# Kernel optimization log

Hardware: AMD Instinct MI355X
Metric: run time of the kernel (lower is better)

## Reference

```python
import jax, jax.numpy as jnp
from jax import lax
import numpy as np

B, T, NCLS, D = 64, 2048, 20, 2048
LCS_LEN, FSD_LEN = 64, 32
LAMB1, LAMB2, LAMB3 = 1.0, 5e-5, 8e-5
LAMB_LCS, LAMB_FSD = 0.01, 0.01
FEAT_MARGIN = 50.0
THRES = 0.5
GAMMA = 0.1


def cos_sim(a, b):
    a = a / jnp.linalg.norm(a, axis=1, keepdims=True)
    b = b / jnp.linalg.norm(b, axis=1, keepdims=True)
    return a @ b.T


def dp_fsd(c0, c1):
    # soft-LCS/DTW-style recurrence with maxGamma (soft max) over 3 neighbors
    h = c0.shape[-1] // 2
    m = cos_sim(c0[:, :h], c1[:, :h])  # [L, L]
    g = cos_sim(c0[:, h:], c1[:, h:])  # [L, L]
    L = m.shape[0]

    def row_step(prev_row, mg):
        m_row, g_row = mg
        diag = prev_row[:-1]  # C[i-1, j-1]
        up = prev_row[1:]     # C[i-1, j]

        def col_step(left, xs):  # left = C[i, j-1]
            d, u, mij, gij = xs
            neigh = jnp.stack([d, gij + u, gij + left])
            val = mij + GAMMA * jax.nn.logsumexp(neigh / GAMMA)
            return val, val

        _, row_vals = lax.scan(col_step, jnp.zeros((), m.dtype), (diag, up, m_row, g_row))
        new_row = jnp.concatenate([jnp.zeros((1,), m.dtype), row_vals])
        return new_row, None

    final_row, _ = lax.scan(row_step, jnp.zeros(L + 1, m.dtype), (m, g))
    return final_row[-1]


def dp_lcs(c0, c1):
    s = cos_sim(c0, c1)  # [L, L]
    L = s.shape[0]

    def row_step(prev_row, s_row):
        diag = prev_row[:-1]
        up = prev_row[1:]

        def col_step(left, xs):
            d, u, sij = xs
            val = jnp.where(sij > THRES, d + sij, jnp.maximum(u, left))
            return val, val

        _, row_vals = lax.scan(col_step, jnp.zeros((), s.dtype), (diag, up, s_row))
        return jnp.concatenate([jnp.zeros((1,), s.dtype), row_vals]), None

    final_row, _ = lax.scan(row_step, jnp.zeros(L + 1, s.dtype), s)
    return final_row[-1]


def cls_criterion(p, lab):
    return -jnp.mean(jnp.sum(jnp.log(p + 1e-10) * lab, axis=1))


def forward_once(ai_cls, ac_cls, ab_cls, vlab, att, ai_feat, ac_feat, ab_feat, ai_cas):
    bs = ai_cls.shape[0]
    ones = jnp.ones((bs, 1), ai_cls.dtype)
    zeros = jnp.zeros((bs, 1), ai_cls.dtype)
    inst_lab = jnp.concatenate([vlab, zeros], axis=1)
    cont_lab = jnp.concatenate([vlab, ones], axis=1)
    back_lab = jnp.concatenate([jnp.zeros_like(vlab), ones], axis=1)
    inst_lab = inst_lab / jnp.sum(inst_lab, axis=1, keepdims=True)
    cont_lab = cont_lab / jnp.sum(cont_lab, axis=1, keepdims=True)
    back_lab = back_lab / jnp.sum(back_lab, axis=1, keepdims=True)

    inst_loss = cls_criterion(ai_cls, inst_lab)
    cont_loss = cls_criterion(ac_cls, cont_lab)
    back_loss = cls_criterion(ab_cls, back_lab)

    guide_loss = jnp.mean(jnp.sum(jnp.abs(1.0 - ai_cas[:, :, -1] - lax.stop_gradient(att[:, :, 0])), axis=1))

    n_inst = jnp.linalg.norm(ai_feat, axis=1)
    n_cont = jnp.linalg.norm(ac_feat, axis=1)
    n_back = jnp.linalg.norm(ab_feat, axis=1)
    f1 = jnp.maximum(FEAT_MARGIN - n_inst + n_cont, 0.0)
    f2 = jnp.maximum(FEAT_MARGIN - n_cont + n_back, 0.0)
    f3 = n_back
    feat_loss = jnp.mean((f1 + f2 + f3) ** 2)

    sparse_loss = jnp.mean(jnp.sum(att[:, :, :2], axis=1))

    cls_loss = inst_loss + cont_loss + back_loss  # THUMOS14 weights 1/1/1
    return cls_loss + LAMB1 * guide_loss + LAMB2 * feat_loss + LAMB3 * sparse_loss


def _pair_loss(vals, pair_label):
    bs = vals.shape[0]
    pos = jnp.sum(vals * pair_label)
    neg = jnp.sum(vals * (1.0 - pair_label))
    pos_num = jnp.sum(pair_label)
    neg_num = bs - pos_num
    return neg / (neg_num + 1e-10) - pos / (pos_num + 1e-10)


def ftcl_forward(act_inst_cls_0, act_cont_cls_0, act_back_cls_0, vid_label_0, temp_att_0,
                 act_inst_feat_0, act_cont_feat_0, act_back_feat_0, act_inst_cas_0,
                 lcs_candi_0, fsd_act_candi_0, fsd_bak_candi_0,
                 act_inst_cls_1, act_cont_cls_1, act_back_cls_1, vid_label_1, temp_att_1,
                 act_inst_feat_1, act_cont_feat_1, act_back_feat_1, act_inst_cas_1,
                 lcs_candi_1, fsd_act_candi_1, fsd_bak_candi_1):
    loss_0 = forward_once(act_inst_cls_0, act_cont_cls_0, act_back_cls_0, vid_label_0, temp_att_0,
                          act_inst_feat_0, act_cont_feat_0, act_back_feat_0, act_inst_cas_0)
    loss_1 = forward_once(act_inst_cls_1, act_cont_cls_1, act_back_cls_1, vid_label_1, temp_att_1,
                          act_inst_feat_1, act_cont_feat_1, act_back_feat_1, act_inst_cas_1)
    acm_loss = (loss_0 + loss_1) / 2.0

    pair_label = (jnp.sum(vid_label_0 * vid_label_1, axis=1) > 0).astype(jnp.float32)  # [B]

    lcs = jax.vmap(dp_lcs)(lcs_candi_0, lcs_candi_1)  # [B]
    lcs_loss = _pair_loss(lcs, pair_label)

    # pair==1 -> act_1, pair==0 -> bak_1 (matches the per-sample branch in torch)
    fsd_c1 = jnp.where(pair_label[:, None, None] > 0, fsd_act_candi_1, fsd_bak_candi_1)
    fsd = jax.vmap(dp_fsd)(fsd_act_candi_0, fsd_c1)  # [B]
    fsd_loss = _pair_loss(fsd, pair_label)

    return acm_loss + LAMB_LCS * lcs_loss + LAMB_FSD * fsd_loss


def setup_inputs() -> dict:
    key = jax.random.key(0)
    ks = iter(jax.random.split(key, 32))
    rand = lambda s: jax.random.uniform(next(ks), s, jnp.float32)
    randn = lambda s: jax.random.normal(next(ks), s, jnp.float32)
    inp = {}
    for sfx in ('0', '1'):
        inp[f'act_inst_cls_{sfx}'] = rand((B, NCLS + 1))
        inp[f'act_cont_cls_{sfx}'] = rand((B, NCLS + 1))
        inp[f'act_back_cls_{sfx}'] = rand((B, NCLS + 1))
        inp[f'vid_label_{sfx}'] = jnp.ones((B, NCLS), jnp.float32)
        inp[f'temp_att_{sfx}'] = rand((B, T, 3))
        inp[f'act_inst_feat_{sfx}'] = randn((B, D))
        inp[f'act_cont_feat_{sfx}'] = randn((B, D))
        inp[f'act_back_feat_{sfx}'] = randn((B, D))
        inp[f'act_inst_cas_{sfx}'] = rand((B, T, NCLS + 1))
        inp[f'lcs_candi_{sfx}'] = randn((B, LCS_LEN, D))
        inp[f'fsd_act_candi_{sfx}'] = randn((B, FSD_LEN, D))
        inp[f'fsd_bak_candi_{sfx}'] = randn((B, FSD_LEN, D))
    return inp


def reference(act_inst_cls_0, act_cont_cls_0, act_back_cls_0, vid_label_0, temp_att_0,
              act_inst_feat_0, act_cont_feat_0, act_back_feat_0, act_inst_cas_0,
              lcs_candi_0, fsd_act_candi_0, fsd_bak_candi_0,
              act_inst_cls_1, act_cont_cls_1, act_back_cls_1, vid_label_1, temp_att_1,
              act_inst_feat_1, act_cont_feat_1, act_back_feat_1, act_inst_cas_1,
              lcs_candi_1, fsd_act_candi_1, fsd_bak_candi_1):
    return ftcl_forward(act_inst_cls_0, act_cont_cls_0, act_back_cls_0, vid_label_0, temp_att_0,
                        act_inst_feat_0, act_cont_feat_0, act_back_feat_0, act_inst_cas_0,
                        lcs_candi_0, fsd_act_candi_0, fsd_bak_candi_0,
                        act_inst_cls_1, act_cont_cls_1, act_back_cls_1, vid_label_1, temp_att_1,
                        act_inst_feat_1, act_cont_feat_1, act_back_feat_1, act_inst_cas_1,
                        lcs_candi_1, fsd_act_candi_1, fsd_bak_candi_1)
```

## Files before the change

kernel.cpp:

```cpp
#include <hip/hip_runtime.h>
#include <math.h>

#define Bn 64
#define Tn 2048
#define NCLS 20
#define Dn 2048
#define LCSL 64
#define FSDL 32

typedef __bf16 bf16x4 __attribute__((ext_vector_type(4)));
typedef __bf16 bf16x8 __attribute__((ext_vector_type(8)));
typedef float f32x4 __attribute__((ext_vector_type(4)));

#define WS_LCS 0
#define WS_FSD 64
#define WS_NORM 128
#define WS_GS 512
template <int NS>
struct WsOff {
    static constexpr size_t LSQ = 1024;
    static constexpr size_t FSQ = LSQ + (size_t)64 * NS * 128;
    static constexpr size_t SPART = FSQ + (size_t)64 * NS * 64;
    static constexpr size_t MG = SPART + (size_t)64 * NS * 4096;
    static constexpr size_t END = MG + (size_t)64 * NS * 1024;
};

template <int NS>
__global__ __launch_bounds__(256) void mega_kernel(
    const float* __restrict__ lcs0, const float* __restrict__ lcs1,
    const float* __restrict__ fA0, const float* __restrict__ fA1,
    const float* __restrict__ fB1,
    const float* __restrict__ vid0, const float* __restrict__ vid1,
    const float* __restrict__ cas0, const float* __restrict__ att0,
    const float* __restrict__ cas1, const float* __restrict__ att1,
    const float* __restrict__ f0, const float* __restrict__ f1,
    const float* __restrict__ f2, const float* __restrict__ f3,
    const float* __restrict__ f4, const float* __restrict__ f5,
    float* __restrict__ ws) {
    constexpr int L = (NS == 16) ? 4 : 3;
    constexpr int KC = 2048 / NS / 64;
    using O = WsOff<NS>;
    __shared__ __align__(16) __bf16 tA[2][4096];
    __shared__ __align__(16) __bf16 tB[2][4096];
    const int t = threadIdx.x;
    const int bid = blockIdx.x;
    const int w = t >> 6, lane = t & 63;
    const int quad = lane >> 4, l16 = lane & 15;

    if (bid < 64 * NS) {
        const int b = bid >> L, ks = bid & (NS - 1);
        const float* c0 = lcs0 + (size_t)b * LCSL * Dn + ks * (2048 / NS);
        const float* c1 = lcs1 + (size_t)b * LCSL * Dn + ks * (2048 / NS);

        f32x4 acc[4] = {};
        float sqa[4] = {0.f, 0.f, 0.f, 0.f}, sqb[4] = {0.f, 0.f, 0.f, 0.f};
        float4 pA[4], pB[4];

        auto LOADL = [&](int st) {
            #pragma unroll
            for (int l = 0; l < 4; ++l) {
                int idx4 = l * 256 + t;
                int row = idx4 >> 4, kq4 = idx4 & 15;
                pA[l] = *(const float4*)(c0 + (size_t)row * Dn + st * 64 + kq4 * 4);
                pB[l] = *(const float4*)(c1 + (size_t)row * Dn + st * 64 + kq4 * 4);
            }
        };
        auto WRITEL = [&](int buf) {
            #pragma unroll
            for (int l = 0; l < 4; ++l) {
                int idx4 = l * 256 + t;
                int row = idx4 >> 4, kq4 = idx4 & 15;
                int c = kq4 >> 1, h = kq4 & 1;
                int pos = row * 64 + ((c ^ (row & 7)) << 3) + h * 4;
                float4 av = pA[l], bv = pB[l];
                bf16x4 a4 = {(__bf16)av.x, (__bf16)av.y, (__bf16)av.z, (__bf16)av.w};
                bf16x4 b4 = {(__bf16)bv.x, (__bf16)bv.y, (__bf16)bv.z, (__bf16)bv.w};
                *(bf16x4*)&tA[buf][pos] = a4;
                *(bf16x4*)&tB[buf][pos] = b4;
                sqa[l] += av.x * av.x + av.y * av.y + av.z * av.z + av.w * av.w;
                sqb[l] += bv.x * bv.x + bv.y * bv.y + bv.z * bv.z + bv.w * bv.w;
            }
        };

        LOADL(0);
        WRITEL(0);
        if (KC > 1) LOADL(1);
        __syncthreads();
        for (int kc = 0; kc < KC; ++kc) {
            const int cur = kc & 1;
            #pragma unroll
            for (int s = 0; s < 2; ++s) {
                int ar = w * 16 + l16;
                int ac_ = (s * 4 + quad) ^ (ar & 7);
                bf16x8 af = *(const bf16x8*)&tA[cur][ar * 64 + (ac_ << 3)];
                #pragma unroll
                for (int tj = 0; tj < 4; ++tj) {
                    int br = tj * 16 + l16;
                    int bc = (s * 4 + quad) ^ (br & 7);
                    bf16x8 bf = *(const bf16x8*)&tB[cur][br * 64 + (bc << 3)];
                    acc[tj] = __builtin_amdgcn_mfma_f32_16x16x32_bf16(af, bf, acc[tj], 0, 0, 0);
                }
            }
            if (kc + 1 < KC) {
                WRITEL(cur ^ 1);
                if (kc + 2 < KC) LOADL(kc + 2);
                __syncthreads();
            }
        }
        float* dst = ws + O::SPART + (size_t)(b * NS + ks) * 4096;
        #pragma unroll
        for (int tj = 0; tj < 4; ++tj)
            #pragma unroll
            for (int rg = 0; rg < 4; ++rg)
                dst[(w * 16 + quad * 4 + rg) * 64 + tj * 16 + l16] = acc[tj][rg];
        #pragma unroll
        for (int l = 0; l < 4; ++l) {
            float sa = sqa[l], sb = sqb[l];
            #pragma unroll
            for (int m = 1; m < 16; m <<= 1) {
                sa += __shfl_xor(sa, m);
                sb += __shfl_xor(sb, m);
            }
            if ((t & 15) == 0) {
                int r = l * 16 + (t >> 4);
                float* q = ws + O::LSQ + (size_t)(b * NS + ks) * 128;
                q[r] = sa;
                q[64 + r] = sb;
            }
        }
    } else if (bid < 128 * NS) {
        const int qb = bid - 64 * NS;
        const int b = qb >> L;
        const int idx = qb & (NS - 1);
        const int half = idx >> (L - 1);
        const int ks = idx & (NS / 2 - 1);
        float ps = 0.f;
        for (int c = 0; c < NCLS; ++c) ps += vid0[b * NCLS + c] * vid1[b * NCLS + c];
        const float* base1 = (ps > 0.f) ? fA1 : fB1;
        const float* c0 = fA0 + (size_t)b * FSDL * Dn + half * 1024 + ks * (2048 / NS);
        const float* c1 = base1 + (size_t)b * FSDL * Dn + half * 1024 + ks * (2048 / NS);
        const int wi = w >> 1, wj = w & 1;

        f32x4 acc = {};
        float sqa[2] = {0.f, 0.f}, sqb[2] = {0.f, 0.f};
        float4 pA[2], pB[2];

        auto LOADF = [&](int st) {
            #pragma unroll
            for (int l = 0; l < 2; ++l) {
                int idx4 = l * 256 + t;
                int row = idx4 >> 4, kq4 = idx4 & 15;
                pA[l] = *(const float4*)(c0 + (size_t)row * Dn + st * 64 + kq4 * 4);
                pB[l] = *(const float4*)(c1 + (size_t)row * Dn + st * 64 + kq4 * 4);
            }
        };
        auto WRITEF = [&](int buf) {
            #pragma unroll
            for (int l = 0; l < 2; ++l) {
                int idx4 = l * 256 + t;
                int row = idx4 >> 4, kq4 = idx4 & 15;
                int c = kq4 >> 1, h = kq4 & 1;
                int pos = row * 64 + ((c ^ (row & 7)) << 3) + h * 4;
                float4 av = pA[l], bv = pB[l];
                bf16x4 a4 = {(__bf16)av.x, (__bf16)av.y, (__bf16)av.z, (__bf16)av.w};
                bf16x4 b4 = {(__bf16)bv.x, (__bf16)bv.y, (__bf16)bv.z, (__bf16)bv.w};
                *(bf16x4*)&tA[buf][pos] = a4;
                *(bf16x4*)&tB[buf][pos] = b4;
                sqa[l] += av.x * av.x + av.y * av.y + av.z * av.z + av.w * av.w;
                sqb[l] += bv.x * bv.x + bv.y * bv.y + bv.z * bv.z + bv.w * bv.w;
            }
        };

        LOADF(0);
        WRITEF(0);
        if (KC > 1) LOADF(1);
        __syncthreads();
        for (int kc = 0; kc < KC; ++kc) {
            const int cur = kc & 1;
            #pragma unroll
            for (int s = 0; s < 2; ++s) {
                int ar = wi * 16 + l16;
                int ac_ = (s * 4 + quad) ^ (ar & 7);
                bf16x8 af = *(const bf16x8*)&tA[cur][ar * 64 + (ac_ << 3)];
                int br = wj * 16 + l16;
                int bc = (s * 4 + quad) ^ (br & 7);
                bf16x8 bf = *(const bf16x8*)&tB[cur][br * 64 + (bc << 3)];
                acc = __builtin_amdgcn_mfma_f32_16x16x32_bf16(af, bf, acc, 0, 0, 0);
            }
            if (kc + 1 < KC) {
                WRITEF(cur ^ 1);
                if (kc + 2 < KC) LOADF(kc + 2);
                __syncthreads();
            }
        }
        float* dst = ws + O::MG + (size_t)((b * 2 + half) * (NS / 2) + ks) * 1024;
        #pragma unroll
        for (int rg = 0; rg < 4; ++rg)
            dst[(wi * 16 + quad * 4 + rg) * 32 + wj * 16 + l16] = acc[rg];
        #pragma unroll
        for (int l = 0; l < 2; ++l) {
            float sa = sqa[l], sb = sqb[l];
            #pragma unroll
            for (int m = 1; m < 16; m <<= 1) {
                sa += __shfl_xor(sa, m);
                sb += __shfl_xor(sb, m);
            }
            if ((t & 15) == 0) {
                int r = l * 16 + (t >> 4);
                float* qq = ws + O::FSQ + (size_t)((b * 2 + half) * (NS / 2) + ks) * 64;
                qq[r] = sa;
                qq[32 + r] = sb;
            }
        }
    } else if (bid < 128 * NS + 128) {
        const int gb = bid - 128 * NS;
        const int N = Bn * Tn;
        float g0 = 0.f, s0 = 0.f, g1 = 0.f, s1 = 0.f;
        for (int n = gb * 256 + t; n < 2 * N; n += 128 * 256) {
            int sfx = (n >= N);
            int m = sfx ? (n - N) : n;
            const float* cas = sfx ? cas1 : cas0;
            const float* att = sfx ? att1 : att0;
            float a0 = att[m * 3 + 0];
            float a1 = att[m * 3 + 1];
            float g = fabsf(1.0f - cas[m * (NCLS + 1) + NCLS] - a0);
            float s = a0 + a1;
            if (sfx) { g1 += g; s1 += s; } else { g0 += g; s0 += s; }
        }
        float* red = (float*)tA;
        float vals[4] = {g0, s0, g1, s1};
        #pragma unroll
        for (int v = 0; v < 4; ++v) red[v * 256 + t] = vals[v];
        __syncthreads();
        for (int o = 128; o; o >>= 1) {
            if (t < o) {
                #pragma unroll
                for (int v = 0; v < 4; ++v) red[v * 256 + t] += red[v * 256 + t + o];
            }
            __syncthreads();
        }
        if (t < 4) ws[WS_GS + gb * 4 + t] = red[t * 256];
    } else {
        int R = (bid - (128 * NS + 128)) * 4 + w;
        const float* arr[6] = {f0, f1, f2, f3, f4, f5};
        const float* p = arr[R >> 6] + (size_t)(R & 63) * Dn;
        float s = 0.f;
        #pragma unroll
        for (int qd = 0; qd < 8; ++qd) {
            float4 v = *(const float4*)(p + qd * 256 + lane * 4);
            s += v.x * v.x + v.y * v.y + v.z * v.z + v.w * v.w;
        }
        for (int off = 32; off; off >>= 1) s += __shfl_down(s, off);
        if (lane == 0) ws[WS_NORM + R] = sqrtf(s);
    }
}

template <int NS>
__global__ __launch_bounds__(256) void dp_kernel(float* __restrict__ ws) {
    using O = WsOff<NS>;
    const int t = threadIdx.x;
    if (blockIdx.x < 64) {
        const int b = blockIdx.x;
        __shared__ float S[64 * 68];
        __shared__ float inv[128];
        if (t < 128) {
            float s = 0.f;
            #pragma unroll
            for (int ks = 0; ks < NS; ++ks)
                s += ws[O::LSQ + (size_t)(b * NS + ks) * 128 + t];
            inv[t] = 1.0f / sqrtf(s);
        }
        __syncthreads();
        const float* sp = ws + O::SPART + (size_t)b * NS * 4096;
        #pragma unroll
        for (int qd = 0; qd < 4; ++qd) {
            int idx4 = qd * 256 + t;
            int i = idx4 >> 4, j = (idx4 & 15) * 4;
            float4 v = {0.f, 0.f, 0.f, 0.f};
            #pragma unroll
            for (int ks = 0; ks < NS; ++ks) {
                float4 p = *(const float4*)(sp + (size_t)ks * 4096 + idx4 * 4);
                v.x += p.x; v.y += p.y; v.z += p.z; v.w += p.w;
            }
            float ri = inv[i];
            S[i * 68 + j + 0] = v.x * ri * inv[64 + j + 0];
            S[i * 68 + j + 1] = v.y * ri * inv[64 + j + 1];
            S[i * 68 + j + 2] = v.z * ri * inv[64 + j + 2];
            S[i * 68 + j + 3] = v.w * ri * inv[64 + j + 3];
        }
        __syncthreads();
        if (t < 64) {
            float prev = 0.f, prevprev = 0.f;
            float sval_next = S[t * 68 + 0];
            for (int d = 2; d <= 128; ++d) {
                float s = sval_next;
                int jn = d - t - 1;
                if (jn >= 0 && jn < 64) sval_next = S[t * 68 + jn];
                float up = __shfl_up(prev, 1);
                float dg = __shfl_up(prevprev, 1);
                if (t == 0) { up = 0.f; dg = 0.f; }
                int j = d - t - 1;
                float left = prev;
                float val = (s > 0.5f) ? (dg + s) : fmaxf(up, left);
                float cur = (j >= 1 && j <= 64) ? val : 0.f;
                prevprev = prev;
                prev = cur;
            }
            if (t == 63) ws[WS_LCS + b] = prev;
        }
    } else {
        const int b = blockIdx.x - 64;
        __shared__ float M[32 * 36], G[32 * 36];
        __shared__ float inv[128];
        if (t < 128) {
            int half = t >> 6, sub = t & 63;
            float s = 0.f;
            #pragma unroll
            for (int ks = 0; ks < NS / 2; ++ks)
                s += ws[O::FSQ + (size_t)((b * 2 + half) * (NS / 2) + ks) * 64 + sub];
            inv[t] = 1.0f / sqrtf(s);
        }
        __syncthreads();
        {
            int idx4 = t;
            int i = idx4 >> 3, j = (idx4 & 7) * 4;
            float4 vM = {0.f, 0.f, 0.f, 0.f}, vG = {0.f, 0.f, 0.f, 0.f};
            #pragma unroll
            for (int ks = 0; ks < NS / 2; ++ks) {
                float4 pM = *(const float4*)(ws + O::MG + (size_t)((b * 2 + 0) * (NS / 2) + ks) * 1024 + idx4 * 4);
                float4 pG = *(const float4*)(ws + O::MG + (size_t)((b * 2 + 1) * (NS / 2) + ks) * 1024 + idx4 * 4);
                vM.x += pM.x; vM.y += pM.y; vM.z += pM.z; vM.w += pM.w;
                vG.x += pG.x; vG.y += pG.y; vG.z += pG.z; vG.w += pG.w;
            }
            float riM = inv[i], riG = inv[64 + i];
            M[i * 36 + j + 0] = vM.x * riM * inv[32 + j + 0];
            M[i * 36 + j + 1] = vM.y * riM * inv[32 + j + 1];
            M[i * 36 + j + 2] = vM.z * riM * inv[32 + j + 2];
            M[i * 36 + j + 3] = vM.w * riM * inv[32 + j + 3];
            G[i * 36 + j + 0] = vG.x * riG * inv[96 + j + 0];
            G[i * 36 + j + 1] = vG.y * riG * inv[96 + j + 1];
            G[i * 36 + j + 2] = vG.z * riG * inv[96 + j + 2];
            G[i * 36 + j + 3] = vG.w * riG * inv[96 + j + 3];
        }
        __syncthreads();
        if (t < 32) {
            float prev = 0.f, prevprev = 0.f;
            float m_next = M[t * 36 + 0], g_next = G[t * 36 + 0];
            for (int d = 2; d <= 64; ++d) {
                float m = m_next, g = g_next;
                int jn = d - t - 1;
                if (jn >= 0 && jn < 32) { m_next = M[t * 36 + jn]; g_next = G[t * 36 + jn]; }
                float up = __shfl_up(prev, 1);
                float dg = __shfl_up(prevprev, 1);
                if (t == 0) { up = 0.f; dg = 0.f; }
                int j = d - t - 1;
                float left = prev;
                float x0 = dg * 10.0f;
                float x1 = (g + up) * 10.0f;
                float x2 = (g + left) * 10.0f;
                float mx = fmaxf(x0, fmaxf(x1, x2));
                float lse = mx + __logf(__expf(x0 - mx) + __expf(x1 - mx) + __expf(x2 - mx));
                float val = m + 0.1f * lse;
                float cur = (j >= 1 && j <= 32) ? val : 0.f;
                prevprev = prev;
                prev = cur;
            }
            if (t == 31) ws[WS_FSD + b] = prev;
        }
    }
}

__device__ __forceinline__ float4 block_reduce4(float4 v, float4* red, int t) {
    red[t] = v;
    __syncthreads();
    for (int o = 128; o; o >>= 1) {
        if (t < o) {
            red[t].x += red[t + o].x;
            red[t].y += red[t + o].y;
            red[t].z += red[t + o].z;
            red[t].w += red[t + o].w;
        }
        __syncthreads();
    }
    float4 r = red[0];
    __syncthreads();
    return r;
}

__global__ __launch_bounds__(256) void final_kernel(
    const float* __restrict__ ai0, const float* __restrict__ ac0,
    const float* __restrict__ ab0, const float* __restrict__ vid0,
    const float* __restrict__ ai1, const float* __restrict__ ac1,
    const float* __restrict__ ab1, const float* __restrict__ vid1,
    const float* __restrict__ ws, float* __restrict__ out) {
    __shared__ float rs0[Bn], rs1[Bn], plsh[Bn];
    __shared__ __align__(16) float4 red[256];
    int t = threadIdx.x;
    if (t < Bn) {
        float s0 = 0.f, s1 = 0.f, pp = 0.f;
        for (int c = 0; c < NCLS; ++c) {
            float a = vid0[t * NCLS + c], bl = vid1[t * NCLS + c];
            s0 += a; s1 += bl; pp += a * bl;
        }
        rs0[t] = s0;
        rs1[t] = s1;
        plsh[t] = (pp > 0.f) ? 1.f : 0.f;
    }
    __syncthreads();

    float inst0 = 0.f, cont0 = 0.f, back0 = 0.f;
    float inst1 = 0.f, cont1 = 0.f, back1 = 0.f;
    for (int idx = t; idx < Bn * (NCLS + 1); idx += 256) {
        int b = idx / (NCLS + 1), c = idx % (NCLS + 1);
        float v0 = (c < NCLS) ? vid0[b * NCLS + c] : 0.f;
        float v1 = (c < NCLS) ? vid1[b * NCLS + c] : 0.f;
        float wI0 = (c < NCLS) ? (v0 / rs0[b]) : 0.f;
        float wC0 = ((c < NCLS) ? v0 : 1.f) / (rs0[b] + 1.f);
        float wI1 = (c < NCLS) ? (v1 / rs1[b]) : 0.f;
        float wC1 = ((c < NCLS) ? v1 : 1.f) / (rs1[b] + 1.f);
        inst0 += logf(ai0[idx] + 1e-10f) * wI0;
        cont0 += logf(ac0[idx] + 1e-10f) * wC0;
        inst1 += logf(ai1[idx] + 1e-10f) * wI1;
        cont1 += logf(ac1[idx] + 1e-10f) * wC1;
        if (c == NCLS) {
            back0 += logf(ab0[idx] + 1e-10f);
            back1 += logf(ab1[idx] + 1e-10f);
        }
    }

    float g0 = 0.f, s0v = 0.f, g1 = 0.f, s1v = 0.f;
    for (int i = t; i < 128; i += 256) {
        g0  += ws[WS_GS + i * 4 + 0];
        s0v += ws[WS_GS + i * 4 + 1];
        g1  += ws[WS_GS + i * 4 + 2];
        s1v += ws[WS_GS + i * 4 + 3];
    }

    float fv0 = 0.f, fv1 = 0.f;
    if (t < Bn) {
        const float* nm = ws + WS_NORM;
        {
            float ni = nm[0 * Bn + t], nc = nm[1 * Bn + t], nb = nm[2 * Bn + t];
            float f1 = fmaxf(50.0f - ni + nc, 0.f);
            float f2 = fmaxf(50.0f - nc + nb, 0.f);
            float f = f1 + f2 + nb;
            fv0 = f * f;
        }
        {
            float ni = nm[3 * Bn + t], nc = nm[4 * Bn + t], nb = nm[5 * Bn + t];
            float f1 = fmaxf(50.0f - ni + nc, 0.f);
            float f2 = fmaxf(50.0f - nc + nb, 0.f);
            float f = f1 + f2 + nb;
            fv1 = f * f;
        }
    }

    float posL = 0.f, negL = 0.f, posF = 0.f, negF = 0.f, pln = 0.f;
    if (t < Bn) {
        float pl = plsh[t];
        float lv = ws[WS_LCS + t];
        float fv = ws[WS_FSD + t];
        posL = lv * pl; negL = lv * (1.f - pl);
        posF = fv * pl; negF = fv * (1.f - pl);
        pln = pl;
    }

    float4 r1 = block_reduce4({inst0, cont0, back0, inst1}, red, t);
    float4 r2 = block_reduce4({cont1, back1, g0, s0v}, red, t);
    float4 r3 = block_reduce4({g1, s1v, fv0, fv1}, red, t);
    float4 r4 = block_reduce4({posL, negL, posF, negF}, red, t);
    float4 r5 = block_reduce4({pln, 0.f, 0.f, 0.f}, red, t);

    if (t == 0) {
        float cls0 = -(r1.x + r1.y + r1.z) / (float)Bn;
        float cls1 = -(r1.w + r2.x + r2.y) / (float)Bn;
        float guide0 = r2.z / (float)Bn;
        float sparse0 = r2.w / (float)(Bn * 2);
        float guide1 = r3.x / (float)Bn;
        float sparse1 = r3.y / (float)(Bn * 2);
        float sFeat0 = r3.z / (float)Bn;
        float sFeat1 = r3.w / (float)Bn;
        float loss0 = cls0 + 1.0f * guide0 + 5e-05f * sFeat0 + 8e-05f * sparse0;
        float loss1 = cls1 + 1.0f * guide1 + 5e-05f * sFeat1 + 8e-05f * sparse1;
        float acm = 0.5f * (loss0 + loss1);
        float posn = r5.x;
        float negn = (float)Bn - posn;
        float lcs_loss = r4.y / (negn + 1e-10f) - r4.x / (posn + 1e-10f);
        float fsd_loss = r4.w / (negn + 1e-10f) - r4.z / (posn + 1e-10f);
        out[0] = acm + 0.01f * lcs_loss + 0.01f * fsd_loss;
    }
}

extern "C" void kernel_launch(void* const* d_in, const int* in_sizes, int n_in,
                              void* d_out, int out_size, void* d_ws, size_t ws_size,
                              hipStream_t stream) {
    (void)in_sizes; (void)n_in; (void)out_size;
    const float* ai0  = (const float*)d_in[0];
    const float* ac0  = (const float*)d_in[1];
    const float* ab0  = (const float*)d_in[2];
    const float* vid0 = (const float*)d_in[3];
    const float* att0 = (const float*)d_in[4];
    const float* fi0  = (const float*)d_in[5];
    const float* fc0  = (const float*)d_in[6];
    const float* fb0  = (const float*)d_in[7];
    const float* cas0 = (const float*)d_in[8];
    const float* lcs0 = (const float*)d_in[9];
    const float* fsdA0 = (const float*)d_in[10];
    const float* ai1  = (const float*)d_in[12];
    const float* ac1  = (const float*)d_in[13];
    const float* ab1  = (const float*)d_in[14];
    const float* vid1 = (const float*)d_in[15];
    const float* att1 = (const float*)d_in[16];
    const float* fi1  = (const float*)d_in[17];
    const float* fc1  = (const float*)d_in[18];
    const float* fb1  = (const float*)d_in[19];
    const float* cas1 = (const float*)d_in[20];
    const float* lcs1 = (const float*)d_in[21];
    const float* fsdA1 = (const float*)d_in[22];
    const float* fsdB1 = (const float*)d_in[23];

    float* ws = (float*)d_ws;

    if (ws_size >= WsOff<16>::END * sizeof(float)) {
        mega_kernel<16><<<128 * 16 + 224, 256, 0, stream>>>(
            lcs0, lcs1, fsdA0, fsdA1, fsdB1, vid0, vid1, cas0, att0, cas1, att1,
            fi0, fc0, fb0, fi1, fc1, fb1, ws);
        dp_kernel<16><<<128, 256, 0, stream>>>(ws);
    } else {
        mega_kernel<8><<<128 * 8 + 224, 256, 0, stream>>>(
            lcs0, lcs1, fsdA0, fsdA1, fsdB1, vid0, vid1, cas0, att0, cas1, att1,
            fi0, fc0, fb0, fi1, fc1, fb1, ws);
        dp_kernel<8><<<128, 256, 0, stream>>>(ws);
    }
    final_kernel<<<1, 256, 0, stream>>>(ai0, ac0, ab0, vid0, ai1, ac1, ab1, vid1, ws,
                                        (float*)d_out);
}
```

Before: 236.0 us.

## Fuse DP into mega kernel with one block per batch, dropping split-K partials

Replaces the split-K scheme (many blocks writing partial similarity tiles to workspace, then a separate dp_kernel reducing them) with one 512-thread block per batch item. Each block computes the full-K similarity GEMM, normalizes it, and runs the DP recurrence in-block. This removes one kernel launch and the workspace round trip for the partial sums. The cost is far less parallelism: 304 blocks instead of over 2000, each looping over the full K dimension, and the FSD path leaves half its waves idle during the MFMA loop. The final kernel's block reductions also switch to wave shuffles.

```diff
diff --git a/kernel.cpp b/kernel.cpp
--- a/kernel.cpp
+++ b/kernel.cpp
@@ -16,17 +16,11 @@
 #define WS_FSD 64
 #define WS_NORM 128
 #define WS_GS 512
-template <int NS>
-struct WsOff {
-    static constexpr size_t LSQ = 1024;
-    static constexpr size_t FSQ = LSQ + (size_t)64 * NS * 128;
-    static constexpr size_t SPART = FSQ + (size_t)64 * NS * 64;
-    static constexpr size_t MG = SPART + (size_t)64 * NS * 4096;
-    static constexpr size_t END = MG + (size_t)64 * NS * 1024;
-};
-
-template <int NS>
-__global__ __launch_bounds__(256) void mega_kernel(
+
+#define AUXB 176
+#define NBLK 304
+
+__global__ __launch_bounds__(512) void mega_kernel(
     const float* __restrict__ lcs0, const float* __restrict__ lcs1,
     const float* __restrict__ fA0, const float* __restrict__ fA1,
     const float* __restrict__ fB1,
@@ -37,29 +31,69 @@
     const float* __restrict__ f2, const float* __restrict__ f3,
     const float* __restrict__ f4, const float* __restrict__ f5,
     float* __restrict__ ws) {
-    constexpr int L = (NS == 16) ? 4 : 3;
-    constexpr int KC = 2048 / NS / 64;
-    using O = WsOff<NS>;
     __shared__ __align__(16) __bf16 tA[2][4096];
     __shared__ __align__(16) __bf16 tB[2][4096];
+    __shared__ __align__(16) float S[64 * 68];
+    __shared__ float inv[128];
     const int t = threadIdx.x;
     const int bid = blockIdx.x;
     const int w = t >> 6, lane = t & 63;
     const int quad = lane >> 4, l16 = lane & 15;
 
-    if (bid < 64 * NS) {
-        const int b = bid >> L, ks = bid & (NS - 1);
-        const float* c0 = lcs0 + (size_t)b * LCSL * Dn + ks * (2048 / NS);
-        const float* c1 = lcs1 + (size_t)b * LCSL * Dn + ks * (2048 / NS);
-
-        f32x4 acc[4] = {};
-        float sqa[4] = {0.f, 0.f, 0.f, 0.f}, sqb[4] = {0.f, 0.f, 0.f, 0.f};
-        float4 pA[4], pB[4];
+    if (bid < 128) {
+        const int gb = bid;
+        const int N = Bn * Tn;
+        float g0 = 0.f, s0 = 0.f, g1 = 0.f, s1 = 0.f;
+        for (int n = gb * 512 + t; n < 2 * N; n += 128 * 512) {
+            int sfx = (n >= N);
+            int m = sfx ? (n - N) : n;
+            const float* cas = sfx ? cas1 : cas0;
+            const float* att = sfx ? att1 : att0;
+            float a0 = att[m * 3 + 0];
+            float a1 = att[m * 3 + 1];
+            float g = fabsf(1.0f - cas[m * (NCLS + 1) + NCLS] - a0);
+            float s = a0 + a1;
+            if (sfx) { g1 += g; s1 += s; } else { g0 += g; s0 += s; }
+        }
+        float* red = S;
+        float vals[4] = {g0, s0, g1, s1};
+        #pragma unroll
+        for (int v = 0; v < 4; ++v) red[v * 512 + t] = vals[v];
+        __syncthreads();
+        for (int o = 256; o; o >>= 1) {
+            if (t < o) {
+                #pragma unroll
+                for (int v = 0; v < 4; ++v) red[v * 512 + t] += red[v * 512 + t + o];
+            }
+            __syncthreads();
+        }
+        if (t < 4) ws[WS_GS + gb * 4 + t] = red[t * 512];
+    } else if (bid < AUXB) {
+        int R = (bid - 128) * 8 + w;
+        const float* arr[6] = {f0, f1, f2, f3, f4, f5};
+        const float* p = arr[R >> 6] + (size_t)(R & 63) * Dn;
+        float s = 0.f;
+        #pragma unroll
+        for (int qd = 0; qd < 8; ++qd) {
+            float4 v = *(const float4*)(p + qd * 256 + lane * 4);
+            s += v.x * v.x + v.y * v.y + v.z * v.z + v.w * v.w;
+        }
+        for (int off = 32; off; off >>= 1) s += __shfl_down(s, off);
+        if (lane == 0) ws[WS_NORM + R] = sqrtf(s);
+    } else if (bid < 240) {
+        const int b = bid - AUXB;
+        const float* c0 = lcs0 + (size_t)b * LCSL * Dn;
+        const float* c1 = lcs1 + (size_t)b * LCSL * Dn;
+        constexpr int KC = 32;
+
+        f32x4 acc[2] = {};
+        float sqa[2] = {0.f, 0.f}, sqb[2] = {0.f, 0.f};
+        float4 pA[2], pB[2];
 
         auto LOADL = [&](int st) {
             #pragma unroll
-            for (int l = 0; l < 4; ++l) {
-                int idx4 = l * 256 + t;
+            for (int l = 0; l < 2; ++l) {
+                int idx4 = l * 512 + t;
                 int row = idx4 >> 4, kq4 = idx4 & 15;
                 pA[l] = *(const float4*)(c0 + (size_t)row * Dn + st * 64 + kq4 * 4);
                 pB[l] = *(const float4*)(c1 + (size_t)row * Dn + st * 64 + kq4 * 4);
@@ -67,8 +101,8 @@
         };
         auto WRITEL = [&](int buf) {
             #pragma unroll
-            for (int l = 0; l < 4; ++l) {
-                int idx4 = l * 256 + t;
+            for (int l = 0; l < 2; ++l) {
+                int idx4 = l * 512 + t;
                 int row = idx4 >> 4, kq4 = idx4 & 15;
                 int c = kq4 >> 1, h = kq4 & 1;
                 int pos = row * 64 + ((c ^ (row & 7)) << 3) + h * 4;
@@ -84,18 +118,18 @@
 
         LOADL(0);
         WRITEL(0);
-        if (KC > 1) LOADL(1);
+        LOADL(1);
         __syncthreads();
         for (int kc = 0; kc < KC; ++kc) {
             const int cur = kc & 1;
             #pragma unroll
             for (int s = 0; s < 2; ++s) {
-                int ar = w * 16 + l16;
+                int ar = (w >> 1) * 16 + l16;
                 int ac_ = (s * 4 + quad) ^ (ar & 7);
                 bf16x8 af = *(const bf16x8*)&tA[cur][ar * 64 + (ac_ << 3)];
                 #pragma unroll
-                for (int tj = 0; tj < 4; ++tj) {
-                    int br = tj * 16 + l16;
+                for (int tj = 0; tj < 2; ++tj) {
+                    int br = (w & 1) * 32 + tj * 16 + l16;
                     int bc = (s * 4 + quad) ^ (br & 7);
                     bf16x8 bf = *(const bf16x8*)&tB[cur][br * 64 + (bc << 3)];
                     acc[tj] = __builtin_amdgcn_mfma_f32_16x16x32_bf16(af, bf, acc[tj], 0, 0, 0);
@@ -107,96 +141,6 @@
                 __syncthreads();
             }
         }
-        float* dst = ws + O::SPART + (size_t)(b * NS + ks) * 4096;
-        #pragma unroll
-        for (int tj = 0; tj < 4; ++tj)
-            #pragma unroll
-            for (int rg = 0; rg < 4; ++rg)
-                dst[(w * 16 + quad * 4 + rg) * 64 + tj * 16 + l16] = acc[tj][rg];
-        #pragma unroll
-        for (int l = 0; l < 4; ++l) {
-            float sa = sqa[l], sb = sqb[l];
-            #pragma unroll
-            for (int m = 1; m < 16; m <<= 1) {
-                sa += __shfl_xor(sa, m);
-                sb += __shfl_xor(sb, m);
-            }
-            if ((t & 15) == 0) {
-                int r = l * 16 + (t >> 4);
-                float* q = ws + O::LSQ + (size_t)(b * NS + ks) * 128;
-                q[r] = sa;
-                q[64 + r] = sb;
-            }
-        }
-    } else if (bid < 128 * NS) {
-        const int qb = bid - 64 * NS;
-        const int b = qb >> L;
-        const int idx = qb & (NS - 1);
-        const int half = idx >> (L - 1);
-        const int ks = idx & (NS / 2 - 1);
-        float ps = 0.f;
-        for (int c = 0; c < NCLS; ++c) ps += vid0[b * NCLS + c] * vid1[b * NCLS + c];
-        const float* base1 = (ps > 0.f) ? fA1 : fB1;
-        const float* c0 = fA0 + (size_t)b * FSDL * Dn + half * 1024 + ks * (2048 / NS);
-        const float* c1 = base1 + (size_t)b * FSDL * Dn + half * 1024 + ks * (2048 / NS);
-        const int wi = w >> 1, wj = w & 1;
-
-        f32x4 acc = {};
-        float sqa[2] = {0.f, 0.f}, sqb[2] = {0.f, 0.f};
-        float4 pA[2], pB[2];
-
-        auto LOADF = [&](int st) {
-            #pragma unroll
-            for (int l = 0; l < 2; ++l) {
-                int idx4 = l * 256 + t;
-                int row = idx4 >> 4, kq4 = idx4 & 15;
-                pA[l] = *(const float4*)(c0 + (size_t)row * Dn + st * 64 + kq4 * 4);
-                pB[l] = *(const float4*)(c1 + (size_t)row * Dn + st * 64 + kq4 * 4);
-            }
-        };
-        auto WRITEF = [&](int buf) {
-            #pragma unroll
-            for (int l = 0; l < 2; ++l) {
-                int idx4 = l * 256 + t;
-                int row = idx4 >> 4, kq4 = idx4 & 15;
-                int c = kq4 >> 1, h = kq4 & 1;
-                int pos = row * 64 + ((c ^ (row & 7)) << 3) + h * 4;
-                float4 av = pA[l], bv = pB[l];
-                bf16x4 a4 = {(__bf16)av.x, (__bf16)av.y, (__bf16)av.z, (__bf16)av.w};
-                bf16x4 b4 = {(__bf16)bv.x, (__bf16)bv.y, (__bf16)bv.z, (__bf16)bv.w};
-                *(bf16x4*)&tA[buf][pos] = a4;
-                *(bf16x4*)&tB[buf][pos] = b4;
-                sqa[l] += av.x * av.x + av.y * av.y + av.z * av.z + av.w * av.w;
-                sqb[l] += bv.x * bv.x + bv.y * bv.y + bv.z * bv.z + bv.w * bv.w;
-            }
-        };
-
-        LOADF(0);
-        WRITEF(0);
-        if (KC > 1) LOADF(1);
-        __syncthreads();
-        for (int kc = 0; kc < KC; ++kc) {
-            const int cur = kc & 1;
-            #pragma unroll
-            for (int s = 0; s < 2; ++s) {
-                int ar = wi * 16 + l16;
-                int ac_ = (s * 4 + quad) ^ (ar & 7);
-                bf16x8 af = *(const bf16x8*)&tA[cur][ar * 64 + (ac_ << 3)];
-                int br = wj * 16 + l16;
-                int bc = (s * 4 + quad) ^ (br & 7);
-                bf16x8 bf = *(const bf16x8*)&tB[cur][br * 64 + (bc << 3)];
-                acc = __builtin_amdgcn_mfma_f32_16x16x32_bf16(af, bf, acc, 0, 0, 0);
-            }
-            if (kc + 1 < KC) {
-                WRITEF(cur ^ 1);
-                if (kc + 2 < KC) LOADF(kc + 2);
-                __syncthreads();
-            }
-        }
-        float* dst = ws + O::MG + (size_t)((b * 2 + half) * (NS / 2) + ks) * 1024;
-        #pragma unroll
-        for (int rg = 0; rg < 4; ++rg)
-            dst[(wi * 16 + quad * 4 + rg) * 32 + wj * 16 + l16] = acc[rg];
         #pragma unroll
         for (int l = 0; l < 2; ++l) {
             float sa = sqa[l], sb = sqb[l];
@@ -206,88 +150,22 @@
                 sb += __shfl_xor(sb, m);
             }
             if ((t & 15) == 0) {
-                int r = l * 16 + (t >> 4);
-                float* qq = ws + O::FSQ + (size_t)((b * 2 + half) * (NS / 2) + ks) * 64;
-                qq[r] = sa;
-                qq[32 + r] = sb;
-            }
-        }
-    } else if (bid < 128 * NS + 128) {
-        const int gb = bid - 128 * NS;
-        const int N = Bn * Tn;
-        float g0 = 0.f, s0 = 0.f, g1 = 0.f, s1 = 0.f;
-        for (int n = gb * 256 + t; n < 2 * N; n += 128 * 256) {
-            int sfx = (n >= N);
-            int m = sfx ? (n - N) : n;
-            const float* cas = sfx ? cas1 : cas0;
-            const float* att = sfx ? att1 : att0;
-            float a0 = att[m * 3 + 0];
-            float a1 = att[m * 3 + 1];
-            float g = fabsf(1.0f - cas[m * (NCLS + 1) + NCLS] - a0);
-            float s = a0 + a1;
-            if (sfx) { g1 += g; s1 += s; } else { g0 += g; s0 += s; }
-        }
-        float* red = (float*)tA;
-        float vals[4] = {g0, s0, g1, s1};
+                int r = l * 32 + (t >> 4);
+                inv[r] = sa;
+                inv[64 + r] = sb;
+            }
+        }
+        __syncthreads();
+        if (t < 128) inv[t] = 1.0f / sqrtf(inv[t]);
+        __syncthreads();
         #pragma unroll
-        for (int v = 0; v < 4; ++v) red[v * 256 + t] = vals[v];
-        __syncthreads();
-        for (int o = 128; o; o >>= 1) {
-            if (t < o) {
-                #pragma unroll
-                for (int v = 0; v < 4; ++v) red[v * 256 + t] += red[v * 256 + t + o];
-            }
-            __syncthreads();
-        }
-        if (t < 4) ws[WS_GS + gb * 4 + t] = red[t * 256];
-    } else {
-        int R = (bid - (128 * NS + 128)) * 4 + w;
-        const float* arr[6] = {f0, f1, f2, f3, f4, f5};
-        const float* p = arr[R >> 6] + (size_t)(R & 63) * Dn;
-        float s = 0.f;
-        #pragma unroll
-        for (int qd = 0; qd < 8; ++qd) {
-            float4 v = *(const float4*)(p + qd * 256 + lane * 4);
-            s += v.x * v.x + v.y * v.y + v.z * v.z + v.w * v.w;
-        }
-        for (int off = 32; off; off >>= 1) s += __shfl_down(s, off);
-        if (lane == 0) ws[WS_NORM + R] = sqrtf(s);
-    }
-}
-
-template <int NS>
-__global__ __launch_bounds__(256) void dp_kernel(float* __restrict__ ws) {
-    using O = WsOff<NS>;
-    const int t = threadIdx.x;
-    if (blockIdx.x < 64) {
-        const int b = blockIdx.x;
-        __shared__ float S[64 * 68];
-        __shared__ float inv[128];
-        if (t < 128) {
-            float s = 0.f;
+        for (int tj = 0; tj < 2; ++tj)
             #pragma unroll
-            for (int ks = 0; ks < NS; ++ks)
-                s += ws[O::LSQ + (size_t)(b * NS + ks) * 128 + t];
-            inv[t] = 1.0f / sqrtf(s);
-        }
-        __syncthreads();
-        const float* sp = ws + O::SPART + (size_t)b * NS * 4096;
-        #pragma unroll
-        for (int qd = 0; qd < 4; ++qd) {
-            int idx4 = qd * 256 + t;
-            int i = idx4 >> 4, j = (idx4 & 15) * 4;
-            float4 v = {0.f, 0.f, 0.f, 0.f};
-            #pragma unroll
-            for (int ks = 0; ks < NS; ++ks) {
-                float4 p = *(const float4*)(sp + (size_t)ks * 4096 + idx4 * 4);
-                v.x += p.x; v.y += p.y; v.z += p.z; v.w += p.w;
-            }
-            float ri = inv[i];
-            S[i * 68 + j + 0] = v.x * ri * inv[64 + j + 0];
-            S[i * 68 + j + 1] = v.y * ri * inv[64 + j + 1];
-            S[i * 68 + j + 2] = v.z * ri * inv[64 + j + 2];
-            S[i * 68 + j + 3] = v.w * ri * inv[64 + j + 3];
-        }
+            for (int rg = 0; rg < 4; ++rg) {
+                int row = (w >> 1) * 16 + quad * 4 + rg;
+                int col = (w & 1) * 32 + tj * 16 + l16;
+                S[row * 68 + col] = acc[tj][rg] * inv[row] * inv[64 + col];
+            }
         __syncthreads();
         if (t < 64) {
             float prev = 0.f, prevprev = 0.f;
@@ -309,47 +187,98 @@
             if (t == 63) ws[WS_LCS + b] = prev;
         }
     } else {
-        const int b = blockIdx.x - 64;
-        __shared__ float M[32 * 36], G[32 * 36];
-        __shared__ float inv[128];
-        if (t < 128) {
-            int half = t >> 6, sub = t & 63;
-            float s = 0.f;
-            #pragma unroll
-            for (int ks = 0; ks < NS / 2; ++ks)
-                s += ws[O::FSQ + (size_t)((b * 2 + half) * (NS / 2) + ks) * 64 + sub];
-            inv[t] = 1.0f / sqrtf(s);
-        }
-        __syncthreads();
-        {
-            int idx4 = t;
-            int i = idx4 >> 3, j = (idx4 & 7) * 4;
-            float4 vM = {0.f, 0.f, 0.f, 0.f}, vG = {0.f, 0.f, 0.f, 0.f};
-            #pragma unroll
-            for (int ks = 0; ks < NS / 2; ++ks) {
-                float4 pM = *(const float4*)(ws + O::MG + (size_t)((b * 2 + 0) * (NS / 2) + ks) * 1024 + idx4 * 4);
-                float4 pG = *(const float4*)(ws + O::MG + (size_t)((b * 2 + 1) * (NS / 2) + ks) * 1024 + idx4 * 4);
-                vM.x += pM.x; vM.y += pM.y; vM.z += pM.z; vM.w += pM.w;
-                vG.x += pG.x; vG.y += pG.y; vG.z += pG.z; vG.w += pG.w;
-            }
-            float riM = inv[i], riG = inv[64 + i];
-            M[i * 36 + j + 0] = vM.x * riM * inv[32 + j + 0];
-            M[i * 36 + j + 1] = vM.y * riM * inv[32 + j + 1];
-            M[i * 36 + j + 2] = vM.z * riM * inv[32 + j + 2];
-            M[i * 36 + j + 3] = vM.w * riM * inv[32 + j + 3];
-            G[i * 36 + j + 0] = vG.x * riG * inv[96 + j + 0];
-            G[i * 36 + j + 1] = vG.y * riG * inv[96 + j + 1];
-            G[i * 36 + j + 2] = vG.z * riG * inv[96 + j + 2];
-            G[i * 36 + j + 3] = vG.w * riG * inv[96 + j + 3];
-        }
-        __syncthreads();
+        const int b = bid - 240;
+        float ps = 0.f;
+        for (int c = 0; c < NCLS; ++c) ps += vid0[b * NCLS + c] * vid1[b * NCLS + c];
+        const float* base1 = (ps > 0.f) ? fA1 : fB1;
+        const float* c0 = fA0 + (size_t)b * FSDL * Dn;
+        const float* c1 = base1 + (size_t)b * FSDL * Dn;
+        const int wi = w >> 1, wj = w & 1;
+        float* Ml = S;
+        float* Gl = S + 1152;
+        constexpr int KC = 16;
+
+        for (int ph = 0; ph < 2; ++ph) {
+            const int off = ph * 1024;
+            f32x4 acc = {};
+            float sqa = 0.f, sqb = 0.f;
+            float4 pA, pB;
+            auto LOADF = [&](int st) {
+                int row = t >> 4, kq4 = t & 15;
+                pA = *(const float4*)(c0 + (size_t)row * Dn + off + st * 64 + kq4 * 4);
+                pB = *(const float4*)(c1 + (size_t)row * Dn + off + st * 64 + kq4 * 4);
+            };
+            auto WRITEF = [&](int buf) {
+                int row = t >> 4, kq4 = t & 15;
+                int c = kq4 >> 1, h = kq4 & 1;
+                int pos = row * 64 + ((c ^ (row & 7)) << 3) + h * 4;
+                float4 av = pA, bv = pB;
+                bf16x4 a4 = {(__bf16)av.x, (__bf16)av.y, (__bf16)av.z, (__bf16)av.w};
+                bf16x4 b4 = {(__bf16)bv.x, (__bf16)bv.y, (__bf16)bv.z, (__bf16)bv.w};
+                *(bf16x4*)&tA[buf][pos] = a4;
+                *(bf16x4*)&tB[buf][pos] = b4;
+                sqa += av.x * av.x + av.y * av.y + av.z * av.z + av.w * av.w;
+                sqb += bv.x * bv.x + bv.y * bv.y + bv.z * bv.z + bv.w * bv.w;
+            };
+
+            LOADF(0);
+            WRITEF(0);
+            LOADF(1);
+            __syncthreads();
+            for (int kc = 0; kc < KC; ++kc) {
+                const int cur = kc & 1;
+                if (w < 4) {
+                    #pragma unroll
+                    for (int s = 0; s < 2; ++s) {
+                        int ar = wi * 16 + l16;
+                        int ac_ = (s * 4 + quad) ^ (ar & 7);
+                        bf16x8 af = *(const bf16x8*)&tA[cur][ar * 64 + (ac_ << 3)];
+                        int br = wj * 16 + l16;
+                        int bc = (s * 4 + quad) ^ (br & 7);
+                        bf16x8 bf = *(const bf16x8*)&tB[cur][br * 64 + (bc << 3)];
+                        acc = __builtin_amdgcn_mfma_f32_16x16x32_bf16(af, bf, acc, 0, 0, 0);
+                    }
+                }
+                if (kc + 1 < KC) {
+                    WRITEF(cur ^ 1);
+                    if (kc + 2 < KC) LOADF(kc + 2);
+                    __syncthreads();
+                }
+            }
+            {
+                float sa = sqa, sb = sqb;
+                #pragma unroll
+                for (int m = 1; m < 16; m <<= 1) {
+                    sa += __shfl_xor(sa, m);
+                    sb += __shfl_xor(sb, m);
+                }
+                if ((t & 15) == 0) {
+                    int r = t >> 4;
+                    inv[r] = sa;
+                    inv[32 + r] = sb;
+                }
+            }
+            __syncthreads();
+            if (t < 64) inv[t] = 1.0f / sqrtf(inv[t]);
+            __syncthreads();
+            if (w < 4) {
+                float* T = (ph == 0) ? Ml : Gl;
+                #pragma unroll
+                for (int rg = 0; rg < 4; ++rg) {
+                    int row = wi * 16 + quad * 4 + rg;
+                    int col = wj * 16 + l16;
+                    T[row * 36 + col] = acc[rg] * inv[row] * inv[32 + col];
+                }
+            }
+            __syncthreads();
+        }
         if (t < 32) {
             float prev = 0.f, prevprev = 0.f;
-            float m_next = M[t * 36 + 0], g_next = G[t * 36 + 0];
+            float m_next = Ml[t * 36 + 0], g_next = Gl[t * 36 + 0];
             for (int d = 2; d <= 64; ++d) {
                 float m = m_next, g = g_next;
                 int jn = d - t - 1;
-                if (jn >= 0 && jn < 32) { m_next = M[t * 36 + jn]; g_next = G[t * 36 + jn]; }
+                if (jn >= 0 && jn < 32) { m_next = Ml[t * 36 + jn]; g_next = Gl[t * 36 + jn]; }
                 float up = __shfl_up(prev, 1);
                 float dg = __shfl_up(prevprev, 1);
                 if (t == 0) { up = 0.f; dg = 0.f; }
@@ -370,19 +299,21 @@
     }
 }
 
-__device__ __forceinline__ float4 block_reduce4(float4 v, float4* red, int t) {
-    red[t] = v;
+__device__ __forceinline__ float4 wbr4(float4 v, float4* redw, int t) {
+    #pragma unroll
+    for (int m = 1; m < 64; m <<= 1) {
+        v.x += __shfl_xor(v.x, m);
+        v.y += __shfl_xor(v.y, m);
+        v.z += __shfl_xor(v.z, m);
+        v.w += __shfl_xor(v.w, m);
+    }
+    if ((t & 63) == 0) redw[t >> 6] = v;
     __syncthreads();
-    for (int o = 128; o; o >>= 1) {
-        if (t < o) {
-            red[t].x += red[t + o].x;
-            red[t].y += red[t + o].y;
-            red[t].z += red[t + o].z;
-            red[t].w += red[t + o].w;
-        }
-        __syncthreads();
-    }
-    float4 r = red[0];
+    float4 r;
+    r.x = redw[0].x + redw[1].x + redw[2].x + redw[3].x;
+    r.y = redw[0].y + redw[1].y + redw[2].y + redw[3].y;
+    r.z = redw[0].z + redw[1].z + redw[2].z + redw[3].z;
+    r.w = redw[0].w + redw[1].w + redw[2].w + redw[3].w;
     __syncthreads();
     return r;
 }
@@ -394,7 +325,7 @@
     const float* __restrict__ ab1, const float* __restrict__ vid1,
     const float* __restrict__ ws, float* __restrict__ out) {
     __shared__ float rs0[Bn], rs1[Bn], plsh[Bn];
-    __shared__ __align__(16) float4 red[256];
+    __shared__ __align__(16) float4 redw[4];
     int t = threadIdx.x;
     if (t < Bn) {
         float s0 = 0.f, s1 = 0.f, pp = 0.f;
@@ -429,11 +360,9 @@
     }
 
     float g0 = 0.f, s0v = 0.f, g1 = 0.f, s1v = 0.f;
-    for (int i = t; i < 128; i += 256) {
-        g0  += ws[WS_GS + i * 4 + 0];
-        s0v += ws[WS_GS + i * 4 + 1];
-        g1  += ws[WS_GS + i * 4 + 2];
-        s1v += ws[WS_GS + i * 4 + 3];
+    if (t < 128) {
+        float4 g = *(const float4*)&ws[WS_GS + t * 4];
+        g0 = g.x; s0v = g.y; g1 = g.z; s1v = g.w;
     }
 
     float fv0 = 0.f, fv1 = 0.f;
@@ -465,11 +394,11 @@
         pln = pl;
     }
 
-    float4 r1 = block_reduce4({inst0, cont0, back0, inst1}, red, t);
-    float4 r2 = block_reduce4({cont1, back1, g0, s0v}, red, t);
-    float4 r3 = block_reduce4({g1, s1v, fv0, fv1}, red, t);
-    float4 r4 = block_reduce4({posL, negL, posF, negF}, red, t);
-    float4 r5 = block_reduce4({pln, 0.f, 0.f, 0.f}, red, t);
+    float4 r1 = wbr4({inst0, cont0, back0, inst1}, redw, t);
+    float4 r2 = wbr4({cont1, back1, g0, s0v}, redw, t);
+    float4 r3 = wbr4({g1, s1v, fv0, fv1}, redw, t);
+    float4 r4 = wbr4({posL, negL, posF, negF}, redw, t);
+    float4 r5 = wbr4({pln, 0.f, 0.f, 0.f}, redw, t);
 
     if (t == 0) {
         float cls0 = -(r1.x + r1.y + r1.z) / (float)Bn;
@@ -494,7 +423,7 @@
 extern "C" void kernel_launch(void* const* d_in, const int* in_sizes, int n_in,
                               void* d_out, int out_size, void* d_ws, size_t ws_size,
                               hipStream_t stream) {
-    (void)in_sizes; (void)n_in; (void)out_size;
+    (void)in_sizes; (void)n_in; (void)out_size; (void)ws_size;
     const float* ai0  = (const float*)d_in[0];
     const float* ac0  = (const float*)d_in[1];
     const float* ab0  = (const float*)d_in[2];
@@ -521,17 +450,9 @@
 
     float* ws = (float*)d_ws;
 
-    if (ws_size >= WsOff<16>::END * sizeof(float)) {
-        mega_kernel<16><<<128 * 16 + 224, 256, 0, stream>>>(
-            lcs0, lcs1, fsdA0, fsdA1, fsdB1, vid0, vid1, cas0, att0, cas1, att1,
-            fi0, fc0, fb0, fi1, fc1, fb1, ws);
-        dp_kernel<16><<<128, 256, 0, stream>>>(ws);
-    } else {
-        mega_kernel<8><<<128 * 8 + 224, 256, 0, stream>>>(
-            lcs0, lcs1, fsdA0, fsdA1, fsdB1, vid0, vid1, cas0, att0, cas1, att1,
-            fi0, fc0, fb0, fi1, fc1, fb1, ws);
-        dp_kernel<8><<<128, 256, 0, stream>>>(ws);
-    }
-    final_kernel<<<1, 256, 0, stream>>>(ai0, ac0, ab0, vid0, ai1, ac1, ab1, vid1, ws,
-                                        (float*)d_out);
+    mega_kernel<<<NBLK, 512, 0, stream>>>(
+        lcs0, lcs1, fsdA0, fsdA1, fsdB1, vid0, vid1, cas0, att0, cas1, att1,
+        fi0, fc0, fb0, fi1, fc1, fb1, ws);
+    final_kernel<<<1, 256, 0, stream>>>(ai0, ac0, ab0, vid0, ai1, ac1, ab1, vid1,
+                                        ws, (float*)d_out);
 }
```

Measured after the change: 227.1 us. 3.7% less time.
